# Kernel tuning notes

Hardware: AMD Instinct MI355X
Metric: run time of the kernel (lower is better)

The kernel has to match this reference:

```python
import jax, jax.numpy as jnp
import numpy as np

B, T, D_MODEL = 1, 2048, 2048
N_HEADS, N_KV_HEADS, HEAD_DIM = 32, 8, 64
N_REP = N_HEADS // N_KV_HEADS
ROPE_THETA = 10000.0


def setup_inputs() -> dict:
    key = jax.random.key(0)
    ks = jax.random.split(key, 5)
    x = jax.random.normal(ks[0], (B, T, D_MODEL), dtype=jnp.float32)
    # rotary frequencies: complex exp stored as (cos, sin) pairs -> [T, HEAD_DIM//2, 2]
    inv_freq = 1.0 / (ROPE_THETA ** (jnp.arange(0, HEAD_DIM, 2, dtype=jnp.float32) / HEAD_DIM))
    angles = jnp.arange(T, dtype=jnp.float32)[:, None] * inv_freq[None, :]  # [T, HEAD_DIM//2]
    freqs_cis = jnp.stack([jnp.cos(angles), jnp.sin(angles)], axis=-1)  # [T, HD/2, 2]
    s = 1.0 / np.sqrt(D_MODEL)
    wq = jax.random.normal(ks[1], (D_MODEL, N_HEADS * HEAD_DIM), dtype=jnp.float32) * s
    wk = jax.random.normal(ks[2], (D_MODEL, N_KV_HEADS * HEAD_DIM), dtype=jnp.float32) * s
    wv = jax.random.normal(ks[3], (D_MODEL, N_KV_HEADS * HEAD_DIM), dtype=jnp.float32) * s
    wo = jax.random.normal(ks[4], (N_HEADS * HEAD_DIM, D_MODEL), dtype=jnp.float32) * (1.0 / np.sqrt(N_HEADS * HEAD_DIM))
    return {"x": x, "freqs_cis": freqs_cis, "wq": wq, "wk": wk, "wv": wv, "wo": wo}


def _apply_rotary(t, freqs_cis):
    # t: [B, T, H, D]; freqs_cis: [T, D//2, 2] as (cos, sin). Complex multiply.
    tr = t.astype(jnp.float32).reshape(*t.shape[:-1], -1, 2)  # [B,T,H,D/2,2]
    re, im = tr[..., 0], tr[..., 1]
    cos = freqs_cis[None, :, None, :, 0]  # [1,T,1,D/2]
    sin = freqs_cis[None, :, None, :, 1]
    out_re = re * cos - im * sin
    out_im = re * sin + im * cos
    out = jnp.stack([out_re, out_im], axis=-1).reshape(t.shape)
    return out.astype(t.dtype)


def reference(x, freqs_cis, wq, wk, wv, wo):
    Bx, Tx, _ = x.shape
    q = (x @ wq).reshape(Bx, Tx, N_HEADS, HEAD_DIM)
    k = (x @ wk).reshape(Bx, Tx, N_KV_HEADS, HEAD_DIM)
    v = (x @ wv).reshape(Bx, Tx, N_KV_HEADS, HEAD_DIM)
    q = _apply_rotary(q, freqs_cis)
    k = _apply_rotary(k, freqs_cis)
    # GQA: group query heads, broadcast against kv heads (no repeat materialization)
    qg = q.transpose(0, 2, 1, 3).reshape(Bx, N_KV_HEADS, N_REP, Tx, HEAD_DIM)  # [B,G,R,T,D]
    kg = k.transpose(0, 2, 1, 3)  # [B,G,T,D]
    vg = v.transpose(0, 2, 1, 3)  # [B,G,T,D]
    scale = 1.0 / np.sqrt(HEAD_DIM)
    scores = jnp.einsum('bgrtd,bgsd->bgrts', qg, kg) * scale  # [B,G,R,T,T]
    causal = jnp.tril(jnp.ones((Tx, Tx), dtype=bool))
    scores = jnp.where(causal, scores, jnp.finfo(scores.dtype).min)
    p = jax.nn.softmax(scores, axis=-1)
    y = jnp.einsum('bgrts,bgsd->bgrtd', p, vg)  # [B,G,R,T,D]
    y = y.reshape(Bx, N_HEADS, Tx, HEAD_DIM).transpose(0, 2, 1, 3).reshape(Bx, Tx, N_HEADS * HEAD_DIM)
    return y @ wo
```

## Files before the change

### kernel.cpp

```cpp
#include <hip/hip_runtime.h>
#include <hip/hip_bf16.h>
#include <stdint.h>
#include <stddef.h>

#define T_SEQ 2048
#define DMODEL 2048
#define NHEADS 32
#define NKV 8
#define HD 64
#define NQD (NHEADS * HD)
#define NKVD (NKV * HD)
#define QKVN (NQD + 2 * NKVD)

typedef __bf16 bf16_t;
typedef __bf16 bf16x8 __attribute__((ext_vector_type(8)));
typedef __bf16 bf16x4 __attribute__((ext_vector_type(4)));
typedef __bf16 bf16x2 __attribute__((ext_vector_type(2)));
typedef float f32x4 __attribute__((ext_vector_type(4)));

typedef __attribute__((address_space(1))) void gvoid_t;
typedef __attribute__((address_space(3))) void lvoid_t;

__device__ __forceinline__ void gload_lds16(const void* g, void* l) {
  __builtin_amdgcn_global_load_lds((gvoid_t*)g, (lvoid_t*)l, 16, 0, 0);
}

__global__ __launch_bounds__(256) void cast_f32_bf16_kernel(
    const float* __restrict__ in, bf16_t* __restrict__ out, int n8) {
  int i = blockIdx.x * 256 + threadIdx.x;
  if (i >= n8) return;
  const float4* p = (const float4*)in + (size_t)i * 2;
  float4 a = p[0], b = p[1];
  bf16x8 o = {(bf16_t)a.x, (bf16_t)a.y, (bf16_t)a.z, (bf16_t)a.w,
              (bf16_t)b.x, (bf16_t)b.y, (bf16_t)b.z, (bf16_t)b.w};
  *(bf16x8*)(out + (size_t)i * 8) = o;
}

__global__ __launch_bounds__(256) void transpose_cast_kernel(
    const float* __restrict__ in, bf16_t* __restrict__ out,
    int R, int C, int ldin, int ldout) {
  __shared__ float tile[32][33];
  const int c0 = blockIdx.x * 32, r0 = blockIdx.y * 32;
  const int tx = threadIdx.x & 31, ty = threadIdx.x >> 5;
#pragma unroll
  for (int i = 0; i < 32; i += 8)
    tile[ty + i][tx] = in[(size_t)(r0 + ty + i) * ldin + c0 + tx];
  __syncthreads();
#pragma unroll
  for (int i = 0; i < 32; i += 8)
    out[(size_t)(c0 + ty + i) * ldout + r0 + tx] = (bf16_t)tile[tx][ty + i];
}

__global__ __launch_bounds__(256) void rope_cast_kernel(
    const float* __restrict__ src, const float* __restrict__ fc,
    bf16_t* __restrict__ dst, int H, int ldin, float oscale) {
  const int i = blockIdx.x * 256 + threadIdx.x;
  const int npr = H * 32;
  const int t = i / npr;
  const int rem = i - t * npr;
  const int h = rem >> 5, fi = rem & 31;
  const float2 rein = *(const float2*)&src[(size_t)t * ldin + h * 64 + fi * 2];
  const float2 cs = *(const float2*)&fc[((size_t)t * 32 + fi) * 2];
  const float o0 = (rein.x * cs.x - rein.y * cs.y) * oscale;
  const float o1 = (rein.x * cs.y + rein.y * cs.x) * oscale;
  bf16x2 ob = {(bf16_t)o0, (bf16_t)o1};
  *(bf16x2*)&dst[(size_t)t * (H * 64) + h * 64 + fi * 2] = ob;
}

__global__ __launch_bounds__(256) void gemm_bt64_kernel(
    const bf16_t* __restrict__ A, const bf16_t* __restrict__ BT,
    float* __restrict__ C, int M, int N, int K) {
  __shared__ bf16_t As[128 * 64];
  __shared__ bf16_t Bs[64 * 64];
  const int tid = threadIdx.x;
  const int lane = tid & 63;
  const int w = tid >> 6;
  const int lr = lane & 15, lg = lane >> 4;
  const int m0 = blockIdx.y * 128, n0 = blockIdx.x * 64;
  const int wm = (w >> 1) * 64, wn = (w & 1) * 32;

  const bf16_t* gA[4];
  bf16_t* lA[4];
#pragma unroll
  for (int j = 0; j < 4; ++j) {
    const int c = tid + j * 256;
    const int row = c >> 3, cc = c & 7;
    gA[j] = A + (size_t)(m0 + row) * K + ((cc ^ (row & 7)) * 8);
    lA[j] = As + c * 8;
  }
  const bf16_t* gB[2];
  bf16_t* lB[2];
#pragma unroll
  for (int j = 0; j < 2; ++j) {
    const int c = tid + j * 256;
    const int row = c >> 3, cc = c & 7;
    gB[j] = BT + (size_t)(n0 + row) * K + ((cc ^ (row & 7)) * 8);
    lB[j] = Bs + c * 8;
  }

  f32x4 acc[4][2] = {};

  for (int k0 = 0; k0 < K; k0 += 64) {
#pragma unroll
    for (int j = 0; j < 4; ++j) gload_lds16(gA[j] + k0, lA[j]);
#pragma unroll
    for (int j = 0; j < 2; ++j) gload_lds16(gB[j] + k0, lB[j]);
    __syncthreads();
#pragma unroll
    for (int ks = 0; ks < 2; ++ks) {
      bf16x8 af[4], bfr[2];
#pragma unroll
      for (int mi = 0; mi < 4; ++mi) {
        const int row = wm + mi * 16 + lr;
        af[mi] = *(const bf16x8*)((const char*)As + row * 128 +
                                  ((ks * 64 + lg * 16) ^ ((row & 7) << 4)));
      }
#pragma unroll
      for (int nj = 0; nj < 2; ++nj) {
        const int row = wn + nj * 16 + lr;
        bfr[nj] = *(const bf16x8*)((const char*)Bs + row * 128 +
                                   ((ks * 64 + lg * 16) ^ ((row & 7) << 4)));
      }
      __builtin_amdgcn_s_setprio(1);
#pragma unroll
      for (int mi = 0; mi < 4; ++mi)
#pragma unroll
        for (int nj = 0; nj < 2; ++nj)
          acc[mi][nj] = __builtin_amdgcn_mfma_f32_16x16x32_bf16(
              af[mi], bfr[nj], acc[mi][nj], 0, 0, 0);
      __builtin_amdgcn_s_setprio(0);
    }
    __syncthreads();
  }

#pragma unroll
  for (int mi = 0; mi < 4; ++mi)
#pragma unroll
    for (int nj = 0; nj < 2; ++nj) {
      const int row = m0 + wm + mi * 16 + lg * 4;
      const int col = n0 + wn + nj * 16 + lr;
#pragma unroll
      for (int r = 0; r < 4; ++r)
        C[(size_t)(row + r) * N + col] = acc[mi][nj][r];
    }
}

__global__ __launch_bounds__(256) void attn_kernel(
    const bf16_t* __restrict__ Q, const bf16_t* __restrict__ Kb,
    const bf16_t* __restrict__ VT, bf16_t* __restrict__ Y) {
  __shared__ bf16_t Ks[2][64 * 64];
  __shared__ bf16_t Vs[2][64 * 64];
  __shared__ char Pb[4][32 * 128];
  const int qt = (int)gridDim.x - 1 - (int)blockIdx.x;
  const int kh = blockIdx.y;
  const int tid = threadIdx.x, lane = tid & 63, w = tid >> 6;
  const int h = kh * 4 + w;
  const int lr = lane & 15, lg = lane >> 4;
  const int q0 = qt * 32;
  char* pb = (char*)Pb[w];
  const int swz = (lr & 7) << 4;

  const int rA = w * 8 + (lane >> 3);
  const int rB = (w + 4) * 8 + (lane >> 3);
  const int ce = (((lane & 7) ^ (lane >> 3)) * 8);
  const bf16_t* kgA = Kb + (size_t)rA * NKVD + kh * HD + ce;
  const bf16_t* kgB = Kb + (size_t)rB * NKVD + kh * HD + ce;
  const bf16_t* vgA = VT + (size_t)(kh * HD + rA) * T_SEQ + ce;
  const bf16_t* vgB = VT + (size_t)(kh * HD + rB) * T_SEQ + ce;
  const int ldA = w * 512 + lane * 8;
  const int ldB = (w + 4) * 512 + lane * 8;

  bf16x8 qf[2][2];
#pragma unroll
  for (int iq = 0; iq < 2; ++iq)
#pragma unroll
    for (int ks = 0; ks < 2; ++ks)
      qf[iq][ks] = *(const bf16x8*)&Q[(size_t)(q0 + iq * 16 + lr) * NQD + h * HD + ks * 32 + lg * 8];

  float m_i[2] = {-1e30f, -1e30f}, l_i[2] = {0.f, 0.f};
  f32x4 acc_o[2][4] = {};

  const int nt = (qt + 2) >> 1;
  gload_lds16(kgA, &Ks[0][ldA]);
  gload_lds16(kgB, &Ks[0][ldB]);
  gload_lds16(vgA, &Vs[0][ldA]);
  gload_lds16(vgB, &Vs[0][ldB]);
  __syncthreads();

  int cur = 0;
  for (int t = 0; t < nt; ++t) {
    const int s0 = t * 64;
    if (t + 1 < nt) {
      const size_t ko = (size_t)(s0 + 64) * NKVD;
      gload_lds16(kgA + ko, &Ks[cur ^ 1][ldA]);
      gload_lds16(kgB + ko, &Ks[cur ^ 1][ldB]);
      gload_lds16(vgA + s0 + 64, &Vs[cur ^ 1][ldA]);
      gload_lds16(vgB + s0 + 64, &Vs[cur ^ 1][ldB]);
    }
    const char* kbase = (const char*)&Ks[cur][0];
    const char* vbase = (const char*)&Vs[cur][0];

    bf16x8 kf[4][2];
#pragma unroll
    for (int j = 0; j < 4; ++j)
#pragma unroll
      for (int ks = 0; ks < 2; ++ks)
        kf[j][ks] = *(const bf16x8*)(kbase + (j * 16 + lr) * 128 + ((ks * 64 + lg * 16) ^ swz));

    f32x4 st[2][4] = {};
    __builtin_amdgcn_s_setprio(1);
#pragma unroll
    for (int iq = 0; iq < 2; ++iq)
#pragma unroll
      for (int j = 0; j < 4; ++j)
#pragma unroll
        for (int ks = 0; ks < 2; ++ks)
          st[iq][j] = __builtin_amdgcn_mfma_f32_16x16x32_bf16(kf[j][ks], qf[iq][ks], st[iq][j], 0, 0, 0);
    __builtin_amdgcn_s_setprio(0);

    bf16x8 vf[2][4];
#pragma unroll
    for (int ks = 0; ks < 2; ++ks)
#pragma unroll
      for (int df = 0; df < 4; ++df)
        vf[ks][df] = *(const bf16x8*)(vbase + (df * 16 + lr) * 128 + ((ks * 64 + lg * 16) ^ swz));

    const bool domask = (s0 + 64 > q0);
#pragma unroll
    for (int iq = 0; iq < 2; ++iq) {
      float sv[16];
      const int tq = q0 + iq * 16 + lr;
#pragma unroll
      for (int j = 0; j < 4; ++j)
#pragma unroll
        for (int r = 0; r < 4; ++r) {
          float v = st[iq][j][r];
          if (domask && (s0 + j * 16 + lg * 4 + r > tq)) v = -1e30f;
          sv[j * 4 + r] = v;
        }
      float pm = fmaxf(fmaxf(fmaxf(sv[0], sv[1]), fmaxf(sv[2], sv[3])),
                       fmaxf(fmaxf(sv[4], sv[5]), fmaxf(sv[6], sv[7])));
      float pm2 = fmaxf(fmaxf(fmaxf(sv[8], sv[9]), fmaxf(sv[10], sv[11])),
                        fmaxf(fmaxf(sv[12], sv[13]), fmaxf(sv[14], sv[15])));
      pm = fmaxf(pm, pm2);
      pm = fmaxf(pm, __shfl_xor(pm, 16));
      pm = fmaxf(pm, __shfl_xor(pm, 32));

      if (!__all(pm <= m_i[iq] + 8.0f)) {
        const float mnew = fmaxf(m_i[iq], pm);
        const float es = exp2f(m_i[iq] - mnew);
        m_i[iq] = mnew;
        l_i[iq] *= es;
        float eso[4];
#pragma unroll
        for (int r = 0; r < 4; ++r) eso[r] = __shfl(es, lg * 4 + r);
#pragma unroll
        for (int df = 0; df < 4; ++df)
#pragma unroll
          for (int r = 0; r < 4; ++r) acc_o[iq][df][r] *= eso[r];
      }

      float rs0 = 0.f, rs1 = 0.f;
      bf16_t pe[16];
#pragma unroll
      for (int z = 0; z < 8; ++z) {
        const float p = exp2f(sv[z] - m_i[iq]);
        rs0 += p;
        pe[z] = (bf16_t)p;
      }
#pragma unroll
      for (int z = 8; z < 16; ++z) {
        const float p = exp2f(sv[z] - m_i[iq]);
        rs1 += p;
        pe[z] = (bf16_t)p;
      }
      l_i[iq] += rs0 + rs1;

#pragma unroll
      for (int j = 0; j < 4; ++j) {
        bf16x4 pk = {pe[j * 4 + 0], pe[j * 4 + 1], pe[j * 4 + 2], pe[j * 4 + 3]};
        *(bf16x4*)(pb + (iq * 16 + lr) * 128 + ((j * 32 + lg * 8) ^ swz)) = pk;
      }
    }

    bf16x8 pa[2][2];
#pragma unroll
    for (int iq = 0; iq < 2; ++iq)
#pragma unroll
      for (int ks = 0; ks < 2; ++ks)
        pa[iq][ks] = *(const bf16x8*)(pb + (iq * 16 + lr) * 128 + ((ks * 64 + lg * 16) ^ swz));

    __builtin_amdgcn_s_setprio(1);
#pragma unroll
    for (int iq = 0; iq < 2; ++iq)
#pragma unroll
      for (int df = 0; df < 4; ++df)
#pragma unroll
        for (int ks = 0; ks < 2; ++ks)
          acc_o[iq][df] = __builtin_amdgcn_mfma_f32_16x16x32_bf16(pa[iq][ks], vf[ks][df], acc_o[iq][df], 0, 0, 0);
    __builtin_amdgcn_s_setprio(0);

    __syncthreads();
    cur ^= 1;
  }

#pragma unroll
  for (int iq = 0; iq < 2; ++iq) {
    float lt = l_i[iq];
    lt += __shfl_xor(lt, 16);
    lt += __shfl_xor(lt, 32);
    float lf[4];
#pragma unroll
    for (int r = 0; r < 4; ++r) lf[r] = __shfl(lt, lg * 4 + r);
#pragma unroll
    for (int r = 0; r < 4; ++r) {
      const float inv = 1.f / lf[r];
      const int t = q0 + iq * 16 + lg * 4 + r;
#pragma unroll
      for (int df = 0; df < 4; ++df)
        Y[(size_t)t * NQD + h * HD + df * 16 + lr] = (bf16_t)(acc_o[iq][df][r] * inv);
    }
  }
}

extern "C" void kernel_launch(void* const* d_in, const int* in_sizes, int n_in,
                              void* d_out, int out_size, void* d_ws, size_t ws_size,
                              hipStream_t stream) {
  const float* x = (const float*)d_in[0];
  const float* fc = (const float*)d_in[1];
  const float* wq = (const float*)d_in[2];
  const float* wk = (const float*)d_in[3];
  const float* wv = (const float*)d_in[4];
  const float* wo = (const float*)d_in[5];
  float* out = (float*)d_out;
  char* ws = (char*)d_ws;

  bf16_t* xb   = (bf16_t*)(ws + 0);
  bf16_t* wT   = (bf16_t*)(ws + (8u << 20));
  float*  qkvf = (float*)(ws + (20u << 20));
  bf16_t* qb   = (bf16_t*)(ws + (8u << 20));
  bf16_t* kb   = (bf16_t*)(ws + (16u << 20));
  bf16_t* vt   = (bf16_t*)(ws + (18u << 20));
  bf16_t* woT  = (bf16_t*)(ws + (20u << 20));
  bf16_t* yb   = (bf16_t*)(ws + (28u << 20));

  const float SCL_Q = 0.18033688011112042f;

  hipLaunchKernelGGL(cast_f32_bf16_kernel, dim3(2048), dim3(256), 0, stream,
                     x, xb, (T_SEQ * DMODEL) / 8);
  hipLaunchKernelGGL(transpose_cast_kernel, dim3(64, 64), dim3(256), 0, stream,
                     wq, wT, DMODEL, NQD, NQD, DMODEL);
  hipLaunchKernelGGL(transpose_cast_kernel, dim3(16, 64), dim3(256), 0, stream,
                     wk, wT + (size_t)NQD * DMODEL, DMODEL, NKVD, NKVD, DMODEL);
  hipLaunchKernelGGL(transpose_cast_kernel, dim3(16, 64), dim3(256), 0, stream,
                     wv, wT + (size_t)(NQD + NKVD) * DMODEL, DMODEL, NKVD, NKVD, DMODEL);
  hipLaunchKernelGGL(gemm_bt64_kernel, dim3(QKVN / 64, T_SEQ / 128), dim3(256), 0, stream,
                     xb, wT, qkvf, T_SEQ, QKVN, DMODEL);
  hipLaunchKernelGGL(rope_cast_kernel, dim3((T_SEQ * NHEADS * 32) / 256), dim3(256), 0, stream,
                     qkvf, fc, qb, NHEADS, QKVN, SCL_Q);
  hipLaunchKernelGGL(rope_cast_kernel, dim3((T_SEQ * NKV * 32) / 256), dim3(256), 0, stream,
                     qkvf + NQD, fc, kb, NKV, QKVN, 1.0f);
  hipLaunchKernelGGL(transpose_cast_kernel, dim3(16, 64), dim3(256), 0, stream,
                     qkvf + NQD + NKVD, vt, T_SEQ, NKVD, QKVN, T_SEQ);
  hipLaunchKernelGGL(transpose_cast_kernel, dim3(64, 64), dim3(256), 0, stream,
                     wo, woT, NQD, DMODEL, DMODEL, NQD);
  hipLaunchKernelGGL(attn_kernel, dim3(T_SEQ / 32, NKV), dim3(256), 0, stream,
                     qb, kb, vt, yb);
  hipLaunchKernelGGL(gemm_bt64_kernel, dim3(DMODEL / 64, T_SEQ / 128), dim3(256), 0, stream,
                     yb, woT, out, T_SEQ, DMODEL, NQD);
}
```

Baseline: 190.2 us.

## Split long causal query tiles across two KV chunks with separate merge kernel

Attention work for the later query tiles (qt>=32) is split into two blocks that each process half of the KV tiles, writing normalized partial outputs plus row max and sum to workspace. A new merge kernel combines the halves with log-sum-exp rescaling. The goal is to balance the causal triangle's uneven per-block work and raise block count from 512 to 768. The cost is an extra launch, partial-output traffic, and bf16 rounding of the partials before merging.

```diff
diff --git a/kernel.cpp b/kernel.cpp
--- a/kernel.cpp
+++ b/kernel.cpp
@@ -147,12 +147,22 @@
 
 __global__ __launch_bounds__(256) void attn_kernel(
     const bf16_t* __restrict__ Q, const bf16_t* __restrict__ Kb,
-    const bf16_t* __restrict__ VT, bf16_t* __restrict__ Y) {
+    const bf16_t* __restrict__ VT, bf16_t* __restrict__ Y,
+    bf16_t* __restrict__ Yp, float* __restrict__ Mb, float* __restrict__ Lb) {
   __shared__ bf16_t Ks[2][64 * 64];
   __shared__ bf16_t Vs[2][64 * 64];
   __shared__ char Pb[4][32 * 128];
-  const int qt = (int)gridDim.x - 1 - (int)blockIdx.x;
-  const int kh = blockIdx.y;
+  const int bid = blockIdx.x;
+  const int kh = bid & 7;
+  const int idx = 95 - (bid >> 3);
+  int qt, c;
+  if (idx < 32) { qt = idx; c = 0; }
+  else { const int t2 = idx - 32; qt = 32 + (t2 >> 1); c = t2 & 1; }
+  const int nt = (qt + 2) >> 1;
+  const bool single = (nt <= 16);
+  const int tstart = c * 16;
+  const int tend = (c == 0) ? (single ? nt : 16) : nt;
+
   const int tid = threadIdx.x, lane = tid & 63, w = tid >> 6;
   const int h = kh * 4 + w;
   const int lr = lane & 15, lg = lane >> 4;
@@ -180,17 +190,19 @@
   float m_i[2] = {-1e30f, -1e30f}, l_i[2] = {0.f, 0.f};
   f32x4 acc_o[2][4] = {};
 
-  const int nt = (qt + 2) >> 1;
-  gload_lds16(kgA, &Ks[0][ldA]);
-  gload_lds16(kgB, &Ks[0][ldB]);
-  gload_lds16(vgA, &Vs[0][ldA]);
-  gload_lds16(vgB, &Vs[0][ldB]);
+  {
+    const size_t ko = (size_t)tstart * 64 * NKVD;
+    gload_lds16(kgA + ko, &Ks[0][ldA]);
+    gload_lds16(kgB + ko, &Ks[0][ldB]);
+    gload_lds16(vgA + tstart * 64, &Vs[0][ldA]);
+    gload_lds16(vgB + tstart * 64, &Vs[0][ldB]);
+  }
   __syncthreads();
 
   int cur = 0;
-  for (int t = 0; t < nt; ++t) {
+  for (int t = tstart; t < tend; ++t) {
     const int s0 = t * 64;
-    if (t + 1 < nt) {
+    if (t + 1 < tend) {
       const size_t ko = (size_t)(s0 + 64) * NKVD;
       gload_lds16(kgA + ko, &Ks[cur ^ 1][ldA]);
       gload_lds16(kgB + ko, &Ks[cur ^ 1][ldB]);
@@ -304,22 +316,78 @@
     cur ^= 1;
   }
 
+  float lts[2];
 #pragma unroll
   for (int iq = 0; iq < 2; ++iq) {
     float lt = l_i[iq];
     lt += __shfl_xor(lt, 16);
     lt += __shfl_xor(lt, 32);
-    float lf[4];
-#pragma unroll
-    for (int r = 0; r < 4; ++r) lf[r] = __shfl(lt, lg * 4 + r);
-#pragma unroll
-    for (int r = 0; r < 4; ++r) {
-      const float inv = 1.f / lf[r];
-      const int t = q0 + iq * 16 + lg * 4 + r;
-#pragma unroll
-      for (int df = 0; df < 4; ++df)
-        Y[(size_t)t * NQD + h * HD + df * 16 + lr] = (bf16_t)(acc_o[iq][df][r] * inv);
-    }
+    lts[iq] = lt;
+  }
+  if (single) {
+#pragma unroll
+    for (int iq = 0; iq < 2; ++iq) {
+      float lf[4];
+#pragma unroll
+      for (int r = 0; r < 4; ++r) lf[r] = __shfl(lts[iq], lg * 4 + r);
+#pragma unroll
+      for (int r = 0; r < 4; ++r) {
+        const float inv = 1.f / lf[r];
+        const int t = q0 + iq * 16 + lg * 4 + r;
+#pragma unroll
+        for (int df = 0; df < 4; ++df)
+          Y[(size_t)t * NQD + h * HD + df * 16 + lr] = (bf16_t)(acc_o[iq][df][r] * inv);
+      }
+    }
+  } else {
+    const int cid = (kh * 32 + (qt - 32)) * 2 + c;
+    bf16_t* yp = Yp + ((size_t)cid * 4 + w) * 2048;
+#pragma unroll
+    for (int iq = 0; iq < 2; ++iq) {
+      float lf[4];
+#pragma unroll
+      for (int r = 0; r < 4; ++r) lf[r] = __shfl(lts[iq], lg * 4 + r);
+#pragma unroll
+      for (int r = 0; r < 4; ++r) {
+        const float inv = 1.f / lf[r];
+        const int q = iq * 16 + lg * 4 + r;
+#pragma unroll
+        for (int df = 0; df < 4; ++df)
+          yp[q * 64 + df * 16 + lr] = (bf16_t)(acc_o[iq][df][r] * inv);
+      }
+    }
+    if (lg == 0) {
+#pragma unroll
+      for (int iq = 0; iq < 2; ++iq) {
+        Mb[cid * 128 + w * 32 + iq * 16 + lr] = m_i[iq];
+        Lb[cid * 128 + w * 32 + iq * 16 + lr] = lts[iq];
+      }
+    }
+  }
+}
+
+__global__ __launch_bounds__(256) void merge_kernel(
+    const bf16_t* __restrict__ Yp, const float* __restrict__ Mb,
+    const float* __restrict__ Lb, bf16_t* __restrict__ Y) {
+  const int qt = 32 + blockIdx.x, kh = blockIdx.y;
+  const int w = threadIdx.x >> 6, lane = threadIdx.x & 63;
+  const int h = kh * 4 + w;
+  const int cid0 = (kh * 32 + (qt - 32)) * 2, cid1 = cid0 + 1;
+  const bf16_t* y0 = Yp + ((size_t)cid0 * 4 + w) * 2048;
+  const bf16_t* y1 = Yp + ((size_t)cid1 * 4 + w) * 2048;
+#pragma unroll 4
+  for (int q = 0; q < 32; ++q) {
+    const float m0 = Mb[cid0 * 128 + w * 32 + q];
+    const float m1 = Mb[cid1 * 128 + w * 32 + q];
+    const float l0 = Lb[cid0 * 128 + w * 32 + q];
+    const float l1 = Lb[cid1 * 128 + w * 32 + q];
+    const float M = fmaxf(m0, m1);
+    const float a0 = exp2f(m0 - M) * l0;
+    const float a1 = exp2f(m1 - M) * l1;
+    const float inv = 1.f / (a0 + a1);
+    const float v0 = (float)y0[q * 64 + lane];
+    const float v1 = (float)y1[q * 64 + lane];
+    Y[(size_t)(qt * 32 + q) * NQD + h * HD + lane] = (bf16_t)((v0 * a0 + v1 * a1) * inv);
   }
 }
 
@@ -342,7 +410,10 @@
   bf16_t* kb   = (bf16_t*)(ws + (16u << 20));
   bf16_t* vt   = (bf16_t*)(ws + (18u << 20));
   bf16_t* woT  = (bf16_t*)(ws + (20u << 20));
-  bf16_t* yb   = (bf16_t*)(ws + (28u << 20));
+  bf16_t* yb   = (bf16_t*)(ws + 0);
+  bf16_t* Yp   = (bf16_t*)(ws + (28u << 20));
+  float*  Mb   = (float*)(ws + (36u << 20));
+  float*  Lb   = (float*)(ws + (36u << 20) + (256u << 10));
 
   const float SCL_Q = 0.18033688011112042f;
 
@@ -364,8 +435,10 @@
                      qkvf + NQD + NKVD, vt, T_SEQ, NKVD, QKVN, T_SEQ);
   hipLaunchKernelGGL(transpose_cast_kernel, dim3(64, 64), dim3(256), 0, stream,
                      wo, woT, NQD, DMODEL, DMODEL, NQD);
-  hipLaunchKernelGGL(attn_kernel, dim3(T_SEQ / 32, NKV), dim3(256), 0, stream,
-                     qb, kb, vt, yb);
+  hipLaunchKernelGGL(attn_kernel, dim3(768), dim3(256), 0, stream,
+                     qb, kb, vt, yb, Yp, Mb, Lb);
+  hipLaunchKernelGGL(merge_kernel, dim3(32, 8), dim3(256), 0, stream,
+                     Yp, Mb, Lb, yb);
   hipLaunchKernelGGL(gemm_bt64_kernel, dim3(DMODEL / 64, T_SEQ / 128), dim3(256), 0, stream,
                      yb, woT, out, T_SEQ, DMODEL, NQD);
 }
```

After: 184.7 us. 2.9% less time.
